# Kernel optimization log

Hardware: AMD Instinct MI355X
Metric: run time of the kernel (lower is better)

Reference implementation:

```python
import jax, jax.numpy as jnp
import numpy as np

# ---- dims (see shape_source) ----
N_NODES = 100_000
N_EDGES = 600_000
N_GRAPHS = 512
N_NODE_FEAT = 90   # atom-type vocabulary
H = 128            # n_hidden_feat
E_FEAT = 256       # n_edge_net_feat
G_FEAT = 128       # n_graph_feat
N_CONV = 3         # n_conv * n_edge_labels, conv_labels = [0,0,0]
SCALE = 0.05


def setup_inputs() -> dict:
    key = jax.random.key(0)
    ks = jax.random.split(key, 16)
    nodes = jax.random.randint(ks[0], (N_NODES,), 0, N_NODE_FEAT)
    edge_sources = jax.random.randint(ks[1], (N_EDGES,), 0, N_NODES)
    edge_targets = jax.random.randint(ks[2], (N_EDGES,), 0, N_NODES)
    graph_indices = jnp.sort(jax.random.randint(ks[3], (N_NODES,), 0, N_GRAPHS))
    node_counts = jnp.maximum(jnp.bincount(graph_indices, length=N_GRAPHS), 1).astype(jnp.float32)

    def rn(k, shape):
        return jax.random.normal(k, shape, jnp.float32) * SCALE

    return {
        "nodes": nodes,
        "edge_sources": edge_sources,
        "edge_targets": edge_targets,
        "graph_indices": graph_indices,
        "node_counts": node_counts,
        # learned parameters
        "embed": rn(ks[4], (N_NODE_FEAT, H)),           # NodeEmbedding table
        "Wg": rn(ks[5], (N_CONV, H, H)),                # gate linear per conv (bias=False)
        "We1": rn(ks[6], (N_CONV, H, E_FEAT)),          # EdgeNetwork layer 1 per conv
        "We2": rn(ks[7], (N_CONV, E_FEAT, H)),          # EdgeNetwork layer 2 per conv
        "Wp": rn(ks[8], (H, H)),                        # LinearPooling
        "Wfc1": rn(ks[9], (H, G_FEAT)), "bfc1": jnp.zeros((G_FEAT,), jnp.float32),
        "Wfc2": rn(ks[10], (G_FEAT, G_FEAT)), "bfc2": jnp.zeros((G_FEAT,), jnp.float32),
        "Wr": rn(ks[11], (G_FEAT, 1)), "br": jnp.zeros((1,), jnp.float32),
    }


def reference(nodes, edge_sources, edge_targets, graph_indices, node_counts,
              embed, Wg, We1, We2, Wp, Wfc1, bfc1, Wfc2, bfc2, Wr, br):
    sp = jax.nn.softplus
    # NodeEmbedding: atom-type lookup -> [N, H]
    x = embed[nodes]
    # Gated graph convolutions: gather -> edge MLP + gate -> scatter-add -> residual
    for i in range(N_CONV):
        z = x[edge_sources]                               # [E, H] gather
        e = sp(z @ We1[i]) @ We2[i]                       # EdgeNetwork (2 layers, no shortcut)
        m = jax.nn.sigmoid(z @ Wg[i]) * sp(e)             # gate * edge_activation(message)
        agg = jax.ops.segment_sum(m, edge_targets, num_segments=N_NODES)  # scatter-add
        x = x + sp(agg)                                   # node_activation + residual
    # LinearPooling (last conv only): per-graph mean of linear(x)
    y = jax.ops.segment_sum(x @ Wp, graph_indices, num_segments=N_GRAPHS) / node_counts[:, None]
    # GraphPooling with n_steps=1: activation only (no batch norm)
    g = sp(y)
    # FullConnection stack (n_fc=2)
    g = sp(g @ Wfc1 + bfc1)
    g = sp(g @ Wfc2 + bfc2)
    return g @ Wr + br
```

## Files before the change

kernel.cpp:

```cpp
#include <hip/hip_runtime.h>
#include <hip/hip_bf16.h>

typedef unsigned short u16;
typedef __attribute__((ext_vector_type(8))) short short8;
typedef __attribute__((ext_vector_type(4))) float f32x4;
typedef __attribute__((ext_vector_type(16))) float f32x16;
typedef __attribute__((ext_vector_type(2))) __bf16 bf16x2;

#define NNODES 100000
#define NEDGES 600000
#define NGRAPHS 512
#define HF 128
#define EF 256
#define GB 32

#define PLD 264
__device__ __forceinline__ int cidx(int chunk, int row){ return chunk * PLD + row * 8; }

__device__ __forceinline__ float bfu(u16 u){ return __uint_as_float(((unsigned)u) << 16); }
__device__ __forceinline__ u16 f2bf(float f){
    unsigned u = __float_as_uint(f);
    unsigned r = (u + 0x7fff + ((u >> 16) & 1)) >> 16;
    return (u16)r;
}
__device__ __forceinline__ unsigned pack2(float a, float b){
    bf16x2 v = { (__bf16)a, (__bf16)b };
    return __builtin_bit_cast(unsigned, v);
}

#if __has_builtin(__builtin_amdgcn_rcpf)
#define RCP1(x) __builtin_amdgcn_rcpf(x)
#else
#define RCP1(x) (1.f / (x))
#endif

__device__ __forceinline__ float sp_f(float x){
    return __logf(1.f + __expf(x));
}
__device__ __forceinline__ float sig_f(float x){
    return RCP1(1.f + __expf(-x));
}
__device__ __forceinline__ float lf(const void* p, long i, bool f32){
    return f32 ? ((const float*)p)[i] : bfu(((const u16*)p)[i]);
}

__device__ __forceinline__ bool is_f32(const void* probe){
    const u16* p = (const u16*)probe;
    int lane = threadIdx.x & 63;
    int c = 0;
#pragma unroll
    for (int i = 0; i < 4; i++) c += (fabsf(bfu(p[lane * 4 + i])) > 1.0f) ? 1 : 0;
#pragma unroll
    for (int off = 32; off; off >>= 1) c += __shfl_xor(c, off, 64);
    return c > 8;
}

__global__ __launch_bounds__(256) void prep_kernel(const void* __restrict__ wg,
                                                   const void* __restrict__ we1,
                                                   const void* __restrict__ we2,
                                                   const void* __restrict__ wp,
                                                   const void* __restrict__ wfc1,
                                                   const void* __restrict__ wfc2,
                                                   u16* __restrict__ pwg,
                                                   u16* __restrict__ pwe1,
                                                   u16* __restrict__ pwe2,
                                                   u16* __restrict__ pwp,
                                                   u16* __restrict__ pf1,
                                                   u16* __restrict__ pf2,
                                                   const void* __restrict__ emb,
                                                   const int* __restrict__ tgt,
                                                   int* __restrict__ counts,
                                                   float* __restrict__ xsum){
    int b = blockIdx.x, t = threadIdx.x;
    if (b < 960) {
        bool f32 = is_f32(emb);
        int i = b * 256 + t;
        int c = i / 81920, r = i % 81920;
        const void* src; u16* dst; int N, KN, l;
        if (r < 16384)      { src = wg;  dst = pwg;  N = HF; KN = 16384; l = r; }
        else if (r < 49152) { src = we1; dst = pwe1; N = EF; KN = 32768; l = r - 16384; }
        else                { src = we2; dst = pwe2; N = HF; KN = 32768; l = r - 49152; }
        int j = l & 7, lane = (l >> 3) & 63, rest = l >> 9;
        int NT = N >> 5;
        int nt = rest % NT, ks = rest / NT;
        int k = ks * 16 + (lane >> 5) * 8 + j;
        int n = nt * 32 + (lane & 31);
        long base = (long)c * KN;
        dst[base + l] = f2bf(lf(src, base + (long)k * N + n, f32));
    } else if (b < 1152) {
        bool f32 = is_f32(emb);
        int i = (b - 960) * 256 + t;
        int c = i / 16384, l = i % 16384;
        const void* src = (c == 0) ? wp : (c == 1) ? wfc1 : wfc2;
        u16* dst = (c == 0) ? pwp : (c == 1) ? pf1 : pf2;
        int j = l & 7, lane = (l >> 3) & 63, rest = l >> 9;
        int nt = rest & 7, kt = rest >> 3;
        int k = kt * 32 + (lane >> 4) * 8 + j;
        int n = nt * 16 + (lane & 15);
        dst[l] = f2bf(lf(src, (long)k * HF + n, f32));
    } else if (b < 3496) {
        int e = (b - 1152) * 256 + t;
        if (e < NEDGES) atomicAdd(&counts[tgt[e]], 1);
    } else {
        int i = (b - 3496) * 256 + t;
        ((float4*)xsum)[i] = make_float4(0.f, 0.f, 0.f, 0.f);
    }
}

__global__ __launch_bounds__(256) void scan1_kernel(const int* __restrict__ counts,
                                                    int* __restrict__ row_ptr,
                                                    int* __restrict__ bsums){
    __shared__ int s[256];
    int t = threadIdx.x;
    int i = blockIdx.x * 256 + t;
    int v = (i < NNODES) ? counts[i] : 0;
    s[t] = v; __syncthreads();
    for (int off = 1; off < 256; off <<= 1) {
        int a = (t >= off) ? s[t - off] : 0;
        __syncthreads();
        s[t] += a;
        __syncthreads();
    }
    if (i < NNODES) row_ptr[i] = s[t] - v;
    if (t == 255) bsums[blockIdx.x] = s[255];
}

__global__ __launch_bounds__(512) void scan2_kernel(const int* __restrict__ bsums,
                                                    int* __restrict__ boffs, int nb){
    __shared__ int s[512];
    int t = threadIdx.x;
    int v = (t < nb) ? bsums[t] : 0;
    s[t] = v; __syncthreads();
    for (int off = 1; off < 512; off <<= 1) {
        int a = (t >= off) ? s[t - off] : 0;
        __syncthreads();
        s[t] += a;
        __syncthreads();
    }
    if (t < nb) boffs[t] = s[t] - v;
}

__global__ __launch_bounds__(256) void scan3_kernel(int* __restrict__ row_ptr,
                                                    const int* __restrict__ boffs,
                                                    int* __restrict__ cursor){
    int i = blockIdx.x * 256 + threadIdx.x;
    if (i < NNODES) {
        int r = row_ptr[i] + boffs[blockIdx.x];
        row_ptr[i] = r;
        cursor[i]  = r;
    }
}

__global__ __launch_bounds__(256) void fill_kernel(const int* __restrict__ src,
                                                   const int* __restrict__ tgt,
                                                   int* __restrict__ cursor,
                                                   int* __restrict__ es){
    int e = blockIdx.x * 256 + threadIdx.x;
    if (e < NEDGES) {
        int pos = atomicAdd(&cursor[tgt[e]], 1);
        es[pos] = src[e];
    }
}

__device__ __forceinline__ void conv_phases(u16* xs, u16* us,
                                            const u16* __restrict__ pwg,
                                            const u16* __restrict__ pwe1,
                                            const u16* __restrict__ pwe2,
                                            u16* __restrict__ M, long row0){
    const int t = threadIdx.x;
    const int w = t >> 6, lane = t & 63;
    const int half = lane >> 5, nn = lane & 31;

    f32x16 acc0 = {}, acc1 = {};
#pragma unroll
    for (int ks = 0; ks < 8; ks++) {
        short8 A0 = *(const short8*)(pwe1 + (((ks * 8 + w) * 64 + lane) << 3));
        short8 A1 = *(const short8*)(pwe1 + (((ks * 8 + w + 4) * 64 + lane) << 3));
        short8 B  = *(const short8*)(&xs[cidx(ks * 2 + half, nn)]);
        acc0 = __builtin_amdgcn_mfma_f32_32x32x16_bf16(A0, B, acc0, 0, 0, 0);
        acc1 = __builtin_amdgcn_mfma_f32_32x32x16_bf16(A1, B, acc1, 0, 0, 0);
    }
#pragma unroll
    for (int q = 0; q < 4; q++) {
        uint2 d;
        d.x = pack2(sp_f(acc0[q*4+0]), sp_f(acc0[q*4+1]));
        d.y = pack2(sp_f(acc0[q*4+2]), sp_f(acc0[q*4+3]));
        *(uint2*)(&us[cidx(w * 4 + q, nn) + half * 4]) = d;
        uint2 e;
        e.x = pack2(sp_f(acc1[q*4+0]), sp_f(acc1[q*4+1]));
        e.y = pack2(sp_f(acc1[q*4+2]), sp_f(acc1[q*4+3]));
        *(uint2*)(&us[cidx(16 + w * 4 + q, nn) + half * 4]) = e;
    }
    __syncthreads();

    f32x16 aT = {};
#pragma unroll
    for (int jj = 0; jj < 16; jj++) {
        short8 Ac = *(const short8*)(pwe2 + (((jj * 4 + w) * 64 + lane) << 3));
        short8 B  = *(const short8*)(&us[cidx(jj * 2 + half, nn)]);
        aT = __builtin_amdgcn_mfma_f32_32x32x16_bf16(Ac, B, aT, 0, 0, 0);
    }

    f32x16 aG = {};
#pragma unroll
    for (int ks = 0; ks < 8; ks++) {
        short8 Ag = *(const short8*)(pwg + (((ks * 4 + w) * 64 + lane) << 3));
        short8 B  = *(const short8*)(&xs[cidx(ks * 2 + half, nn)]);
        aG = __builtin_amdgcn_mfma_f32_32x32x16_bf16(Ag, B, aG, 0, 0, 0);
    }
    long node = row0 + nn;
#pragma unroll
    for (int q = 0; q < 4; q++) {
        int h0 = w * 32 + half * 4 + q * 8;
        uint2 d;
        d.x = pack2(sig_f(aG[q*4+0]) * sp_f(aT[q*4+0]),
                    sig_f(aG[q*4+1]) * sp_f(aT[q*4+1]));
        d.y = pack2(sig_f(aG[q*4+2]) * sp_f(aT[q*4+2]),
                    sig_f(aG[q*4+3]) * sp_f(aT[q*4+3]));
        *(uint2*)(M + node * HF + h0) = d;
    }
}

__global__ __launch_bounds__(256, 6) void conv0_mfma(const int* __restrict__ nodes,
                                                     const void* __restrict__ emb,
                                                     u16* __restrict__ x,
                                                     const u16* __restrict__ pwg,
                                                     const u16* __restrict__ pwe1,
                                                     const u16* __restrict__ pwe2,
                                                     u16* __restrict__ M){
    __shared__ u16 xs[16 * PLD];
    __shared__ u16 us[32 * PLD];
    const int t = threadIdx.x;
    const long row0 = (long)blockIdx.x * 32;
    const bool f32 = is_f32(emb);

    for (int i = t; i < 512; i += 256) {
        int r = i >> 4, q = i & 15;
        long node = row0 + r;
        int v = nodes[node];
        uint4 d;
        if (f32) {
            float4 f0 = ((const float4*)emb)[(long)v * 32 + q * 2];
            float4 f1 = ((const float4*)emb)[(long)v * 32 + q * 2 + 1];
            d.x = pack2(f0.x, f0.y); d.y = pack2(f0.z, f0.w);
            d.z = pack2(f1.x, f1.y); d.w = pack2(f1.z, f1.w);
        } else {
            d = ((const uint4*)emb)[(long)v * 16 + q];
        }
        ((uint4*)x)[node * 16 + q] = d;
        *(uint4*)(&xs[cidx(q, r)]) = d;
    }
    __syncthreads();
    conv_phases(xs, us, pwg, pwe1, pwe2, M, row0);
}

__global__ __launch_bounds__(256, 6) void conv_mfma(const u16* __restrict__ x,
                                                    const u16* __restrict__ pwg,
                                                    const u16* __restrict__ pwe1,
                                                    const u16* __restrict__ pwe2,
                                                    u16* __restrict__ M){
    __shared__ u16 xs[16 * PLD];
    __shared__ u16 us[32 * PLD];
    const int t = threadIdx.x;
    const long row0 = (long)blockIdx.x * 32;

    for (int i = t; i < 512; i += 256) {
        int r = i >> 4, q = i & 15;
        long node = row0 + r;
        uint4 v = ((const uint4*)x)[node * 16 + q];
        *(uint4*)(&xs[cidx(q, r)]) = v;
    }
    __syncthreads();
    conv_phases(xs, us, pwg, pwe1, pwe2, M, row0);
}

__global__ __launch_bounds__(256) void agg_kernel(const u16* __restrict__ M,
                                                  const int* __restrict__ row_ptr,
                                                  const int* __restrict__ counts,
                                                  const int* __restrict__ es,
                                                  u16* __restrict__ x){
    int wid = blockIdx.x * 4 + (threadIdx.x >> 6);
    int lane = threadIdx.x & 63;
    long v = (long)wid * 4 + (lane >> 4);
    int l = lane & 15;
    if (v >= NNODES) return;
    int start = row_ptr[v], cnt = counts[v];
    float a0=0.f,a1=0.f,a2=0.f,a3=0.f,a4=0.f,a5=0.f,a6=0.f,a7=0.f;
    float b0=0.f,b1=0.f,b2=0.f,b3=0.f,b4=0.f,b5=0.f,b6=0.f,b7=0.f;
    const uint4* Mu = (const uint4*)M;
    int e = 0;
    for (; e + 3 < cnt; e += 4) {
        int s0 = es[start + e],     s1 = es[start + e + 1];
        int s2 = es[start + e + 2], s3 = es[start + e + 3];
        uint4 u0 = Mu[(long)s0 * 16 + l];
        uint4 u1 = Mu[(long)s1 * 16 + l];
        uint4 u2 = Mu[(long)s2 * 16 + l];
        uint4 u3 = Mu[(long)s3 * 16 + l];
        a0 += bfu((u16)u0.x); a1 += bfu((u16)(u0.x >> 16));
        a2 += bfu((u16)u0.y); a3 += bfu((u16)(u0.y >> 16));
        a4 += bfu((u16)u0.z); a5 += bfu((u16)(u0.z >> 16));
        a6 += bfu((u16)u0.w); a7 += bfu((u16)(u0.w >> 16));
        b0 += bfu((u16)u1.x); b1 += bfu((u16)(u1.x >> 16));
        b2 += bfu((u16)u1.y); b3 += bfu((u16)(u1.y >> 16));
        b4 += bfu((u16)u1.z); b5 += bfu((u16)(u1.z >> 16));
        b6 += bfu((u16)u1.w); b7 += bfu((u16)(u1.w >> 16));
        a0 += bfu((u16)u2.x); a1 += bfu((u16)(u2.x >> 16));
        a2 += bfu((u16)u2.y); a3 += bfu((u16)(u2.y >> 16));
        a4 += bfu((u16)u2.z); a5 += bfu((u16)(u2.z >> 16));
        a6 += bfu((u16)u2.w); a7 += bfu((u16)(u2.w >> 16));
        b0 += bfu((u16)u3.x); b1 += bfu((u16)(u3.x >> 16));
        b2 += bfu((u16)u3.y); b3 += bfu((u16)(u3.y >> 16));
        b4 += bfu((u16)u3.z); b5 += bfu((u16)(u3.z >> 16));
        b6 += bfu((u16)u3.w); b7 += bfu((u16)(u3.w >> 16));
    }
    for (; e < cnt; e++) {
        int s0 = es[start + e];
        uint4 u0 = Mu[(long)s0 * 16 + l];
        a0 += bfu((u16)u0.x); a1 += bfu((u16)(u0.x >> 16));
        a2 += bfu((u16)u0.y); a3 += bfu((u16)(u0.y >> 16));
        a4 += bfu((u16)u0.z); a5 += bfu((u16)(u0.z >> 16));
        a6 += bfu((u16)u0.w); a7 += bfu((u16)(u0.w >> 16));
    }
    a0 += b0; a1 += b1; a2 += b2; a3 += b3;
    a4 += b4; a5 += b5; a6 += b6; a7 += b7;
    uint4* xu = (uint4*)x;
    uint4 xv = xu[v * 16 + l];
    xv.x = pack2(bfu((u16)xv.x) + sp_f(a0), bfu((u16)(xv.x >> 16)) + sp_f(a1));
    xv.y = pack2(bfu((u16)xv.y) + sp_f(a2), bfu((u16)(xv.y >> 16)) + sp_f(a3));
    xv.z = pack2(bfu((u16)xv.z) + sp_f(a4), bfu((u16)(xv.z >> 16)) + sp_f(a5));
    xv.w = pack2(bfu((u16)xv.w) + sp_f(a6), bfu((u16)(xv.w >> 16)) + sp_f(a7));
    xu[v * 16 + l] = xv;
}

__global__ __launch_bounds__(256) void pool_kernel(const u16* __restrict__ x,
                                                   const int* __restrict__ gidx,
                                                   float* __restrict__ xsum){
    int wave = blockIdx.x * 4 + (threadIdx.x >> 6);
    int lane = threadIdx.x & 63;
    long base = (long)wave * 64;
    if (base >= NNODES) return;
    long end = base + 64; if (end > NNODES) end = NNODES;
    const unsigned* xu = (const unsigned*)x;
    int gcur = gidx[base];
    float a0 = 0.f, a1 = 0.f;
    for (long v = base; v < end; v++) {
        int g = gidx[v];
        if (g != gcur) {
            atomicAdd(&xsum[gcur * HF + lane * 2 + 0], a0);
            atomicAdd(&xsum[gcur * HF + lane * 2 + 1], a1);
            a0 = a1 = 0.f; gcur = g;
        }
        unsigned u = xu[v * 64 + lane];
        a0 += bfu((u16)u);
        a1 += bfu((u16)(u >> 16));
    }
    atomicAdd(&xsum[gcur * HF + lane * 2 + 0], a0);
    atomicAdd(&xsum[gcur * HF + lane * 2 + 1], a1);
}

__global__ __launch_bounds__(256) void head_mfma(const float* __restrict__ xsum,
                                                 const void* __restrict__ ncnt,
                                                 const u16* __restrict__ pwp,
                                                 const u16* __restrict__ pf1,
                                                 const u16* __restrict__ pf2,
                                                 const void* __restrict__ bfc1,
                                                 const void* __restrict__ bfc2,
                                                 const void* __restrict__ Wr,
                                                 const void* __restrict__ br,
                                                 void* __restrict__ out,
                                                 const void* __restrict__ probe){
    __shared__ u16 hibuf[2][GB][136];
    __shared__ u16 lobuf[2][GB][136];
    const int t = threadIdx.x;
    const int w = t >> 6, lane = t & 63;
    const int quad = lane >> 4, nr = lane & 15;
    const bool f32 = is_f32(probe);
    const int g0 = blockIdx.x * GB;

    for (int i = t; i < GB * 64; i += 256) {
        int g = i >> 6, c = (i & 63) * 2;
        float f0 = xsum[(g0 + g) * HF + c], f1 = xsum[(g0 + g) * HF + c + 1];
        u16 h0 = f2bf(f0), h1 = f2bf(f1);
        *(unsigned*)&hibuf[0][g][c] = (unsigned)h0 | ((unsigned)h1 << 16);
        *(unsigned*)&lobuf[0][g][c] = pack2(f0 - bfu(h0), f1 - bfu(h1));
    }
    __syncthreads();

    float rc[2];
#pragma unroll
    for (int nt = 0; nt < 2; nt++) rc[nt] = RCP1(lf(ncnt, g0 + nt * 16 + nr, f32));

    int cur = 0;
    for (int layer = 0; layer < 3; layer++) {
        const u16* pw = (layer == 0) ? pwp : (layer == 1) ? pf1 : pf2;
        const void* bias = (layer == 1) ? bfc1 : bfc2;
        int nxt = cur ^ 1;
#pragma unroll
        for (int c = 0; c < 2; c++) {
            int et = w * 2 + c;
            short8 A[4];
#pragma unroll
            for (int kt = 0; kt < 4; kt++)
                A[kt] = *(const short8*)(pw + (((kt * 8 + et) * 64 + lane) << 3));
#pragma unroll
            for (int nt = 0; nt < 2; nt++) {
                f32x4 acc = {0.f, 0.f, 0.f, 0.f};
#pragma unroll
                for (int kt = 0; kt < 4; kt++) {
                    short8 bh = *(const short8*)(&hibuf[cur][nt * 16 + nr][kt * 32 + quad * 8]);
                    short8 bl = *(const short8*)(&lobuf[cur][nt * 16 + nr][kt * 32 + quad * 8]);
                    acc = __builtin_amdgcn_mfma_f32_16x16x32_bf16(A[kt], bh, acc, 0, 0, 0);
                    acc = __builtin_amdgcn_mfma_f32_16x16x32_bf16(A[kt], bl, acc, 0, 0, 0);
                }
                int feat0 = et * 16 + quad * 4;
                float f[4];
#pragma unroll
                for (int r = 0; r < 4; r++) {
                    float a = (layer == 0) ? acc[r] * rc[nt]
                                           : acc[r] + lf(bias, feat0 + r, f32);
                    f[r] = sp_f(a);
                }
                u16 h[4]; float lo[4];
#pragma unroll
                for (int r = 0; r < 4; r++) { h[r] = f2bf(f[r]); lo[r] = f[r] - bfu(h[r]); }
                uint2 dh, dl;
                dh.x = (unsigned)h[0] | ((unsigned)h[1] << 16);
                dh.y = (unsigned)h[2] | ((unsigned)h[3] << 16);
                dl.x = pack2(lo[0], lo[1]);
                dl.y = pack2(lo[2], lo[3]);
                *(uint2*)&hibuf[nxt][nt * 16 + nr][feat0] = dh;
                *(uint2*)&lobuf[nxt][nt * 16 + nr][feat0] = dl;
            }
        }
        __syncthreads();
        cur = nxt;
    }

    int g = t >> 3, sub = t & 7;
    float p = 0.f;
    for (int k = sub * 16; k < sub * 16 + 16; k++) {
        float v = bfu(hibuf[cur][g][k]) + bfu(lobuf[cur][g][k]);
        p += v * lf(Wr, k, f32);
    }
    p += __shfl_down(p, 4, 64);
    p += __shfl_down(p, 2, 64);
    p += __shfl_down(p, 1, 64);
    if (sub == 0) {
        float res = p + lf(br, 0, f32);
        if (f32) ((float*)out)[g0 + g] = res;
        else     ((u16*)out)[g0 + g]  = f2bf(res);
    }
}

extern "C" void kernel_launch(void* const* d_in, const int* in_sizes, int n_in,
                              void* d_out, int out_size, void* d_ws, size_t ws_size,
                              hipStream_t stream) {
    const int* nodes = (const int*)d_in[0];
    const int* esrc  = (const int*)d_in[1];
    const int* etgt  = (const int*)d_in[2];
    const int* gidx  = (const int*)d_in[3];

    size_t off = 0;
    char* w = (char*)d_ws;
    auto take = [&](size_t bytes) -> void* {
        void* p = w + off;
        off = (off + bytes + 255) & ~(size_t)255;
        return p;
    };

    u16* pwg     = (u16*)take((size_t)3 * HF * HF * 2);
    u16* pwe1    = (u16*)take((size_t)3 * HF * EF * 2);
    u16* pwe2    = (u16*)take((size_t)3 * EF * HF * 2);
    u16* pwp     = (u16*)take((size_t)HF * HF * 2);
    u16* pf1     = (u16*)take((size_t)HF * HF * 2);
    u16* pf2     = (u16*)take((size_t)HF * HF * 2);
    int* counts  = (int*)take((size_t)NNODES * 4);
    int* row_ptr = (int*)take((size_t)NNODES * 4);
    int* cursor  = (int*)take((size_t)NNODES * 4);
    int* es      = (int*)take((size_t)NEDGES * 4);
    int* bsums   = (int*)take(2048);
    int* boffs   = (int*)take(2048);
    float* xsum  = (float*)take((size_t)NGRAPHS * HF * 4);
    u16* x       = (u16*)take((size_t)NNODES * HF * 2);
    u16* M       = (u16*)take((size_t)NNODES * HF * 2);

    hipMemsetAsync(counts, 0, (size_t)NNODES * 4, stream);

    prep_kernel<<<3560, 256, 0, stream>>>(d_in[6], d_in[7], d_in[8],
                                          d_in[9], d_in[10], d_in[12],
                                          pwg, pwe1, pwe2, pwp, pf1, pf2,
                                          d_in[5], etgt, counts, xsum);

    const int NB_SCAN = (NNODES + 255) / 256;
    const int NB_EDGE = (NEDGES + 255) / 256;
    scan1_kernel<<<NB_SCAN, 256, 0, stream>>>(counts, row_ptr, bsums);
    scan2_kernel<<<1, 512, 0, stream>>>(bsums, boffs, NB_SCAN);
    scan3_kernel<<<NB_SCAN, 256, 0, stream>>>(row_ptr, boffs, cursor);
    fill_kernel<<<NB_EDGE, 256, 0, stream>>>(esrc, etgt, cursor, es);

    const int NBC = (NNODES + 31) / 32;
    const int NBA = (NNODES + 15) / 16;
    conv0_mfma<<<NBC, 256, 0, stream>>>(nodes, d_in[5], x, pwg, pwe1, pwe2, M);
    agg_kernel<<<NBA, 256, 0, stream>>>(M, row_ptr, counts, es, x);
    conv_mfma<<<NBC, 256, 0, stream>>>(x,
        pwg + (size_t)1 * HF * HF, pwe1 + (size_t)1 * HF * EF, pwe2 + (size_t)1 * EF * HF, M);
    agg_kernel<<<NBA, 256, 0, stream>>>(M, row_ptr, counts, es, x);
    conv_mfma<<<NBC, 256, 0, stream>>>(x,
        pwg + (size_t)2 * HF * HF, pwe1 + (size_t)2 * HF * EF, pwe2 + (size_t)2 * EF * HF, M);
    agg_kernel<<<NBA, 256, 0, stream>>>(M, row_ptr, counts, es, x);

    pool_kernel<<<(NNODES + 255) / 256, 256, 0, stream>>>(x, gidx, xsum);
    head_mfma<<<NGRAPHS / GB, 256, 0, stream>>>(xsum, d_in[4], pwp, pf1, pf2,
                                                d_in[11], d_in[13], d_in[14], d_in[15],
                                                d_out, d_in[5]);
}
```

Baseline: 392.6 us.

## Make conv kernels persistent with register-resident weights and prefetched node tiles

Measured after the change: 388.0 us. Within noise of the previous version (-1.2%).

```diff
diff --git a/kernel.cpp b/kernel.cpp
--- a/kernel.cpp
+++ b/kernel.cpp
@@ -13,6 +13,8 @@
 #define HF 128
 #define EF 256
 #define GB 32
+#define NTILES 3125
+#define GRID_CONV 512
 
 #define PLD 264
 __device__ __forceinline__ int cidx(int chunk, int row){ return chunk * PLD + row * 8; }
@@ -162,23 +164,33 @@
     }
 }
 
-__device__ __forceinline__ void conv_phases(u16* xs, u16* us,
-                                            const u16* __restrict__ pwg,
-                                            const u16* __restrict__ pwe1,
-                                            const u16* __restrict__ pwe2,
-                                            u16* __restrict__ M, long row0){
-    const int t = threadIdx.x;
-    const int w = t >> 6, lane = t & 63;
+struct ConvW { short8 wu0[8], wu1[8], wc[16], wg[8]; };
+
+__device__ __forceinline__ void load_w(ConvW& W, const u16* __restrict__ pwg,
+                                       const u16* __restrict__ pwe1,
+                                       const u16* __restrict__ pwe2,
+                                       int w, int lane){
+#pragma unroll
+    for (int ks = 0; ks < 8; ks++) {
+        W.wu0[ks] = *(const short8*)(pwe1 + (((ks * 8 + w) * 64 + lane) << 3));
+        W.wu1[ks] = *(const short8*)(pwe1 + (((ks * 8 + w + 4) * 64 + lane) << 3));
+        W.wg[ks]  = *(const short8*)(pwg  + (((ks * 4 + w) * 64 + lane) << 3));
+    }
+#pragma unroll
+    for (int jj = 0; jj < 16; jj++)
+        W.wc[jj] = *(const short8*)(pwe2 + (((jj * 4 + w) * 64 + lane) << 3));
+}
+
+__device__ __forceinline__ void conv_loop1(const ConvW& W, const u16* xs, u16* us,
+                                           int w, int lane, f32x16& aG_out){
     const int half = lane >> 5, nn = lane & 31;
-
-    f32x16 acc0 = {}, acc1 = {};
+    f32x16 acc0 = {}, acc1 = {}, g = {};
 #pragma unroll
     for (int ks = 0; ks < 8; ks++) {
-        short8 A0 = *(const short8*)(pwe1 + (((ks * 8 + w) * 64 + lane) << 3));
-        short8 A1 = *(const short8*)(pwe1 + (((ks * 8 + w + 4) * 64 + lane) << 3));
-        short8 B  = *(const short8*)(&xs[cidx(ks * 2 + half, nn)]);
-        acc0 = __builtin_amdgcn_mfma_f32_32x32x16_bf16(A0, B, acc0, 0, 0, 0);
-        acc1 = __builtin_amdgcn_mfma_f32_32x32x16_bf16(A1, B, acc1, 0, 0, 0);
+        short8 B = *(const short8*)(&xs[cidx(ks * 2 + half, nn)]);
+        acc0 = __builtin_amdgcn_mfma_f32_32x32x16_bf16(W.wu0[ks], B, acc0, 0, 0, 0);
+        acc1 = __builtin_amdgcn_mfma_f32_32x32x16_bf16(W.wu1[ks], B, acc1, 0, 0, 0);
+        g    = __builtin_amdgcn_mfma_f32_32x32x16_bf16(W.wg[ks],  B, g,    0, 0, 0);
     }
 #pragma unroll
     for (int q = 0; q < 4; q++) {
@@ -191,22 +203,18 @@
         e.y = pack2(sp_f(acc1[q*4+2]), sp_f(acc1[q*4+3]));
         *(uint2*)(&us[cidx(16 + w * 4 + q, nn) + half * 4]) = e;
     }
-    __syncthreads();
-
+    aG_out = g;
+}
+
+__device__ __forceinline__ void conv_loop2(const ConvW& W, const u16* us,
+                                           const f32x16& aG, u16* __restrict__ M,
+                                           long row0, int w, int lane){
+    const int half = lane >> 5, nn = lane & 31;
     f32x16 aT = {};
 #pragma unroll
     for (int jj = 0; jj < 16; jj++) {
-        short8 Ac = *(const short8*)(pwe2 + (((jj * 4 + w) * 64 + lane) << 3));
-        short8 B  = *(const short8*)(&us[cidx(jj * 2 + half, nn)]);
-        aT = __builtin_amdgcn_mfma_f32_32x32x16_bf16(Ac, B, aT, 0, 0, 0);
-    }
-
-    f32x16 aG = {};
-#pragma unroll
-    for (int ks = 0; ks < 8; ks++) {
-        short8 Ag = *(const short8*)(pwg + (((ks * 4 + w) * 64 + lane) << 3));
-        short8 B  = *(const short8*)(&xs[cidx(ks * 2 + half, nn)]);
-        aG = __builtin_amdgcn_mfma_f32_32x32x16_bf16(Ag, B, aG, 0, 0, 0);
+        short8 B = *(const short8*)(&us[cidx(jj * 2 + half, nn)]);
+        aT = __builtin_amdgcn_mfma_f32_32x32x16_bf16(W.wc[jj], B, aT, 0, 0, 0);
     }
     long node = row0 + nn;
 #pragma unroll
@@ -221,7 +229,7 @@
     }
 }
 
-__global__ __launch_bounds__(256, 6) void conv0_mfma(const int* __restrict__ nodes,
+__global__ __launch_bounds__(256, 2) void conv0_mfma(const int* __restrict__ nodes,
                                                      const void* __restrict__ emb,
                                                      u16* __restrict__ x,
                                                      const u16* __restrict__ pwg,
@@ -231,30 +239,82 @@
     __shared__ u16 xs[16 * PLD];
     __shared__ u16 us[32 * PLD];
     const int t = threadIdx.x;
-    const long row0 = (long)blockIdx.x * 32;
+    const int w = t >> 6, lane = t & 63;
+    const int r0 = t >> 4, q = t & 15;
     const bool f32 = is_f32(emb);
 
-    for (int i = t; i < 512; i += 256) {
-        int r = i >> 4, q = i & 15;
-        long node = row0 + r;
-        int v = nodes[node];
-        uint4 d;
+    ConvW W;
+    load_w(W, pwg, pwe1, pwe2, w, lane);
+
+    const float4* ef = (const float4*)emb;
+    const uint4*  eu = (const uint4*)emb;
+    uint4* xg = (uint4*)x;
+
+    int tile = blockIdx.x;
+    {
+        long row0 = (long)tile * 32;
+        int v0 = nodes[row0 + r0], v1 = nodes[row0 + r0 + 16];
+        uint4 b0, b1;
         if (f32) {
-            float4 f0 = ((const float4*)emb)[(long)v * 32 + q * 2];
-            float4 f1 = ((const float4*)emb)[(long)v * 32 + q * 2 + 1];
-            d.x = pack2(f0.x, f0.y); d.y = pack2(f0.z, f0.w);
-            d.z = pack2(f1.x, f1.y); d.w = pack2(f1.z, f1.w);
+            float4 f0 = ef[(long)v0 * 32 + q * 2], f1 = ef[(long)v0 * 32 + q * 2 + 1];
+            float4 f2 = ef[(long)v1 * 32 + q * 2], f3 = ef[(long)v1 * 32 + q * 2 + 1];
+            b0.x = pack2(f0.x, f0.y); b0.y = pack2(f0.z, f0.w);
+            b0.z = pack2(f1.x, f1.y); b0.w = pack2(f1.z, f1.w);
+            b1.x = pack2(f2.x, f2.y); b1.y = pack2(f2.z, f2.w);
+            b1.z = pack2(f3.x, f3.y); b1.w = pack2(f3.z, f3.w);
         } else {
-            d = ((const uint4*)emb)[(long)v * 16 + q];
+            b0 = eu[(long)v0 * 16 + q];
+            b1 = eu[(long)v1 * 16 + q];
         }
-        ((uint4*)x)[node * 16 + q] = d;
-        *(uint4*)(&xs[cidx(q, r)]) = d;
+        xg[(row0 + r0) * 16 + q] = b0;
+        xg[(row0 + r0 + 16) * 16 + q] = b1;
+        *(uint4*)(&xs[cidx(q, r0)]) = b0;
+        *(uint4*)(&xs[cidx(q, r0 + 16)]) = b1;
     }
     __syncthreads();
-    conv_phases(xs, us, pwg, pwe1, pwe2, M, row0);
-}
-
-__global__ __launch_bounds__(256, 6) void conv_mfma(const u16* __restrict__ x,
+
+    for (;;) {
+        long row0 = (long)tile * 32;
+        int nxt = tile + GRID_CONV;
+        bool have = nxt < NTILES;
+        uint4 nb0 = {}, nb1 = {};
+        float4 nf0 = {}, nf1 = {}, nf2 = {}, nf3 = {};
+        if (have) {
+            long nr = (long)nxt * 32;
+            int v0 = nodes[nr + r0], v1 = nodes[nr + r0 + 16];
+            if (f32) {
+                nf0 = ef[(long)v0 * 32 + q * 2]; nf1 = ef[(long)v0 * 32 + q * 2 + 1];
+                nf2 = ef[(long)v1 * 32 + q * 2]; nf3 = ef[(long)v1 * 32 + q * 2 + 1];
+            } else {
+                nb0 = eu[(long)v0 * 16 + q];
+                nb1 = eu[(long)v1 * 16 + q];
+            }
+        }
+        f32x16 aG;
+        conv_loop1(W, xs, us, w, lane, aG);
+        __syncthreads();
+        if (have) {
+            uint4 b0 = nb0, b1 = nb1;
+            if (f32) {
+                b0.x = pack2(nf0.x, nf0.y); b0.y = pack2(nf0.z, nf0.w);
+                b0.z = pack2(nf1.x, nf1.y); b0.w = pack2(nf1.z, nf1.w);
+                b1.x = pack2(nf2.x, nf2.y); b1.y = pack2(nf2.z, nf2.w);
+                b1.z = pack2(nf3.x, nf3.y); b1.w = pack2(nf3.z, nf3.w);
+            }
+            long nr = (long)nxt * 32;
+            xg[(nr + r0) * 16 + q] = b0;
+            xg[(nr + r0 + 16) * 16 + q] = b1;
+            *(uint4*)(&xs[cidx(q, r0)]) = b0;
+            *(uint4*)(&xs[cidx(q, r0 + 16)]) = b1;
+        }
+        conv_loop2(W, us, aG, M, row0, w, lane);
+        if (!have) break;
+        __syncthreads();
+        tile = nxt;
+    }
+}
+
+__global__ __launch_bounds__(256, 2) void conv_mfma(const u16* __restrict__ x,
                                                     const u16* __restrict__ pwg,
                                                     const u16* __restrict__ pwe1,
                                                     const u16* __restrict__ pwe2,
@@ -262,16 +322,45 @@
     __shared__ u16 xs[16 * PLD];
     __shared__ u16 us[32 * PLD];
     const int t = threadIdx.x;
-    const long row0 = (long)blockIdx.x * 32;
-
-    for (int i = t; i < 512; i += 256) {
-        int r = i >> 4, q = i & 15;
-        long node = row0 + r;
-        uint4 v = ((const uint4*)x)[node * 16 + q];
-        *(uint4*)(&xs[cidx(q, r)]) = v;
+    const int w = t >> 6, lane = t & 63;
+    const int r0 = t >> 4, q = t & 15;
+
+    ConvW W;
+    load_w(W, pwg, pwe1, pwe2, w, lane);
+
+    const uint4* xg = (const uint4*)x;
+    int tile = blockIdx.x;
+    {
+        long row0 = (long)tile * 32;
+        uint4 b0 = xg[(row0 + r0) * 16 + q];
+        uint4 b1 = xg[(row0 + r0 + 16) * 16 + q];
+        *(uint4*)(&xs[cidx(q, r0)]) = b0;
+        *(uint4*)(&xs[cidx(q, r0 + 16)]) = b1;
     }
     __syncthreads();
-    conv_phases(xs, us, pwg, pwe1, pwe2, M, row0);
+
+    for (;;) {
+        long row0 = (long)tile * 32;
+        int nxt = tile + GRID_CONV;
+        bool have = nxt < NTILES;
+        uint4 nb0 = {}, nb1 = {};
+        if (have) {
+            long nr = (long)nxt * 32;
+            nb0 = xg[(nr + r0) * 16 + q];
+            nb1 = xg[(nr + r0 + 16) * 16 + q];
+        }
+        f32x16 aG;
+        conv_loop1(W, xs, us, w, lane, aG);
+        __syncthreads();
+        if (have) {
+            *(uint4*)(&xs[cidx(q, r0)]) = nb0;
+            *(uint4*)(&xs[cidx(q, r0 + 16)]) = nb1;
+        }
+        conv_loop2(W, us, aG, M, row0, w, lane);
+        if (!have) break;
+        __syncthreads();
+        tile = nxt;
+    }
 }
 
 __global__ __launch_bounds__(256) void agg_kernel(const u16* __restrict__ M,
@@ -498,14 +587,13 @@
     scan3_kernel<<<NB_SCAN, 256, 0, stream>>>(row_ptr, boffs, cursor);
     fill_kernel<<<NB_EDGE, 256, 0, stream>>>(esrc, etgt, cursor, es);
 
-    const int NBC = (NNODES + 31) / 32;
     const int NBA = (NNODES + 15) / 16;
-    conv0_mfma<<<NBC, 256, 0, stream>>>(nodes, d_in[5], x, pwg, pwe1, pwe2, M);
+    conv0_mfma<<<GRID_CONV, 256, 0, stream>>>(nodes, d_in[5], x, pwg, pwe1, pwe2, M);
     agg_kernel<<<NBA, 256, 0, stream>>>(M, row_ptr, counts, es, x);
-    conv_mfma<<<NBC, 256, 0, stream>>>(x,
+    conv_mfma<<<GRID_CONV, 256, 0, stream>>>(x,
         pwg + (size_t)1 * HF * HF, pwe1 + (size_t)1 * HF * EF, pwe2 + (size_t)1 * EF * HF, M);
     agg_kernel<<<NBA, 256, 0, stream>>>(M, row_ptr, counts, es, x);
-    conv_mfma<<<NBC, 256, 0, stream>>>(x,
+    conv_mfma<<<GRID_CONV, 256, 0, stream>>>(x,
         pwg + (size_t)2 * HF * HF, pwe1 + (size_t)2 * HF * EF, pwe2 + (size_t)2 * EF * HF, M);
     agg_kernel<<<NBA, 256, 0, stream>>>(M, row_ptr, counts, es, x);
 
```

## Run conv tiles on a single wave with register-resident activations, no LDS

Applied to the files above, without the earlier changes.

After: 433.4 us. 1.1x slower.

```diff
diff --git a/kernel.cpp b/kernel.cpp
--- a/kernel.cpp
+++ b/kernel.cpp
@@ -13,9 +13,7 @@
 #define HF 128
 #define EF 256
 #define GB 32
-
-#define PLD 264
-__device__ __forceinline__ int cidx(int chunk, int row){ return chunk * PLD + row * 8; }
+#define NTILES 3125
 
 __device__ __forceinline__ float bfu(u16 u){ return __uint_as_float(((unsigned)u) << 16); }
 __device__ __forceinline__ u16 f2bf(float f){
@@ -162,116 +160,118 @@
     }
 }
 
-__device__ __forceinline__ void conv_phases(u16* xs, u16* us,
-                                            const u16* __restrict__ pwg,
-                                            const u16* __restrict__ pwe1,
-                                            const u16* __restrict__ pwe2,
-                                            u16* __restrict__ M, long row0){
-    const int t = threadIdx.x;
-    const int w = t >> 6, lane = t & 63;
-    const int half = lane >> 5, nn = lane & 31;
-
-    f32x16 acc0 = {}, acc1 = {};
-#pragma unroll
-    for (int ks = 0; ks < 8; ks++) {
-        short8 A0 = *(const short8*)(pwe1 + (((ks * 8 + w) * 64 + lane) << 3));
-        short8 A1 = *(const short8*)(pwe1 + (((ks * 8 + w + 4) * 64 + lane) << 3));
-        short8 B  = *(const short8*)(&xs[cidx(ks * 2 + half, nn)]);
-        acc0 = __builtin_amdgcn_mfma_f32_32x32x16_bf16(A0, B, acc0, 0, 0, 0);
-        acc1 = __builtin_amdgcn_mfma_f32_32x32x16_bf16(A1, B, acc1, 0, 0, 0);
-    }
-#pragma unroll
-    for (int q = 0; q < 4; q++) {
-        uint2 d;
-        d.x = pack2(sp_f(acc0[q*4+0]), sp_f(acc0[q*4+1]));
-        d.y = pack2(sp_f(acc0[q*4+2]), sp_f(acc0[q*4+3]));
-        *(uint2*)(&us[cidx(w * 4 + q, nn) + half * 4]) = d;
-        uint2 e;
-        e.x = pack2(sp_f(acc1[q*4+0]), sp_f(acc1[q*4+1]));
-        e.y = pack2(sp_f(acc1[q*4+2]), sp_f(acc1[q*4+3]));
-        *(uint2*)(&us[cidx(16 + w * 4 + q, nn) + half * 4]) = e;
-    }
-    __syncthreads();
-
-    f32x16 aT = {};
-#pragma unroll
-    for (int jj = 0; jj < 16; jj++) {
-        short8 Ac = *(const short8*)(pwe2 + (((jj * 4 + w) * 64 + lane) << 3));
-        short8 B  = *(const short8*)(&us[cidx(jj * 2 + half, nn)]);
-        aT = __builtin_amdgcn_mfma_f32_32x32x16_bf16(Ac, B, aT, 0, 0, 0);
-    }
-
-    f32x16 aG = {};
-#pragma unroll
-    for (int ks = 0; ks < 8; ks++) {
-        short8 Ag = *(const short8*)(pwg + (((ks * 4 + w) * 64 + lane) << 3));
-        short8 B  = *(const short8*)(&xs[cidx(ks * 2 + half, nn)]);
-        aG = __builtin_amdgcn_mfma_f32_32x32x16_bf16(Ag, B, aG, 0, 0, 0);
-    }
-    long node = row0 + nn;
-#pragma unroll
-    for (int q = 0; q < 4; q++) {
-        int h0 = w * 32 + half * 4 + q * 8;
-        uint2 d;
-        d.x = pack2(sig_f(aG[q*4+0]) * sp_f(aT[q*4+0]),
-                    sig_f(aG[q*4+1]) * sp_f(aT[q*4+1]));
-        d.y = pack2(sig_f(aG[q*4+2]) * sp_f(aT[q*4+2]),
-                    sig_f(aG[q*4+3]) * sp_f(aT[q*4+3]));
-        *(uint2*)(M + node * HF + h0) = d;
-    }
-}
-
-__global__ __launch_bounds__(256, 6) void conv0_mfma(const int* __restrict__ nodes,
-                                                     const void* __restrict__ emb,
-                                                     u16* __restrict__ x,
-                                                     const u16* __restrict__ pwg,
-                                                     const u16* __restrict__ pwe1,
-                                                     const u16* __restrict__ pwe2,
-                                                     u16* __restrict__ M){
-    __shared__ u16 xs[16 * PLD];
-    __shared__ u16 us[32 * PLD];
-    const int t = threadIdx.x;
-    const long row0 = (long)blockIdx.x * 32;
-    const bool f32 = is_f32(emb);
-
-    for (int i = t; i < 512; i += 256) {
-        int r = i >> 4, q = i & 15;
-        long node = row0 + r;
-        int v = nodes[node];
-        uint4 d;
-        if (f32) {
-            float4 f0 = ((const float4*)emb)[(long)v * 32 + q * 2];
-            float4 f1 = ((const float4*)emb)[(long)v * 32 + q * 2 + 1];
-            d.x = pack2(f0.x, f0.y); d.y = pack2(f0.z, f0.w);
-            d.z = pack2(f1.x, f1.y); d.w = pack2(f1.z, f1.w);
-        } else {
-            d = ((const uint4*)emb)[(long)v * 16 + q];
-        }
-        ((uint4*)x)[node * 16 + q] = d;
-        *(uint4*)(&xs[cidx(q, r)]) = d;
-    }
-    __syncthreads();
-    conv_phases(xs, us, pwg, pwe1, pwe2, M, row0);
-}
-
-__global__ __launch_bounds__(256, 6) void conv_mfma(const u16* __restrict__ x,
+__device__ __forceinline__ void conv_core(const uint4* xf,
+                                          const u16* __restrict__ pwg,
+                                          const u16* __restrict__ pwe1,
+                                          const u16* __restrict__ pwe2,
+                                          u16* __restrict__ M,
+                                          long node, int lane){
+    const int h = lane >> 5;
+
+    uint4 BU[16];
+#pragma unroll
+    for (int et = 0; et < 8; et++) {
+        f32x16 acc = {};
+#pragma unroll
+        for (int ks = 0; ks < 8; ks++) {
+            short8 A = *(const short8*)(pwe1 + (((ks * 8 + et) * 64 + lane) << 3));
+            acc = __builtin_amdgcn_mfma_f32_32x32x16_bf16(
+                      A, __builtin_bit_cast(short8, xf[ks]), acc, 0, 0, 0);
+        }
+#pragma unroll
+        for (int rb = 0; rb < 2; rb++) {
+            unsigned a1 = pack2(sp_f(acc[rb*8+0]), sp_f(acc[rb*8+1]));
+            unsigned a2 = pack2(sp_f(acc[rb*8+2]), sp_f(acc[rb*8+3]));
+            unsigned b1 = pack2(sp_f(acc[rb*8+4]), sp_f(acc[rb*8+5]));
+            unsigned b2 = pack2(sp_f(acc[rb*8+6]), sp_f(acc[rb*8+7]));
+            unsigned t1 = __shfl_xor(h ? a1 : b1, 32, 64);
+            unsigned t2 = __shfl_xor(h ? a2 : b2, 32, 64);
+            BU[et*2+rb] = make_uint4(h ? t1 : a1, h ? t2 : a2,
+                                     h ? b1 : t1, h ? b2 : t2);
+        }
+    }
+
+#pragma unroll 1
+    for (int ht = 0; ht < 4; ht++) {
+        f32x16 aT = {};
+#pragma unroll
+        for (int jj = 0; jj < 16; jj++) {
+            short8 A = *(const short8*)(pwe2 + (((jj * 4 + ht) * 64 + lane) << 3));
+            aT = __builtin_amdgcn_mfma_f32_32x32x16_bf16(
+                     A, __builtin_bit_cast(short8, BU[jj]), aT, 0, 0, 0);
+        }
+        f32x16 aG = {};
+#pragma unroll
+        for (int ks = 0; ks < 8; ks++) {
+            short8 A = *(const short8*)(pwg + (((ks * 4 + ht) * 64 + lane) << 3));
+            aG = __builtin_amdgcn_mfma_f32_32x32x16_bf16(
+                     A, __builtin_bit_cast(short8, xf[ks]), aG, 0, 0, 0);
+        }
+#pragma unroll
+        for (int q = 0; q < 4; q++) {
+            int h0 = ht * 32 + h * 4 + q * 8;
+            uint2 d;
+            d.x = pack2(sig_f(aG[q*4+0]) * sp_f(aT[q*4+0]),
+                        sig_f(aG[q*4+1]) * sp_f(aT[q*4+1]));
+            d.y = pack2(sig_f(aG[q*4+2]) * sp_f(aT[q*4+2]),
+                        sig_f(aG[q*4+3]) * sp_f(aT[q*4+3]));
+            *(uint2*)(M + node * HF + h0) = d;
+        }
+    }
+}
+
+__global__ __launch_bounds__(64, 2) void conv0_mfma(const int* __restrict__ nodes,
+                                                    const void* __restrict__ emb,
+                                                    u16* __restrict__ x,
                                                     const u16* __restrict__ pwg,
                                                     const u16* __restrict__ pwe1,
                                                     const u16* __restrict__ pwe2,
                                                     u16* __restrict__ M){
-    __shared__ u16 xs[16 * PLD];
-    __shared__ u16 us[32 * PLD];
-    const int t = threadIdx.x;
-    const long row0 = (long)blockIdx.x * 32;
-
-    for (int i = t; i < 512; i += 256) {
-        int r = i >> 4, q = i & 15;
-        long node = row0 + r;
-        uint4 v = ((const uint4*)x)[node * 16 + q];
-        *(uint4*)(&xs[cidx(q, r)]) = v;
-    }
-    __syncthreads();
-    conv_phases(xs, us, pwg, pwe1, pwe2, M, row0);
+    const int lane = threadIdx.x;
+    const int h = lane >> 5, nn = lane & 31;
+    const long node = (long)blockIdx.x * 32 + nn;
+    const bool f32 = is_f32(emb);
+    const int v = nodes[node];
+
+    uint4 xf[8];
+    if (f32) {
+        const float4* ef = (const float4*)emb;
+#pragma unroll
+        for (int ks = 0; ks < 8; ks++) {
+            float4 f0 = ef[(long)v * 32 + ks * 4 + h * 2];
+            float4 f1 = ef[(long)v * 32 + ks * 4 + h * 2 + 1];
+            uint4 d;
+            d.x = pack2(f0.x, f0.y); d.y = pack2(f0.z, f0.w);
+            d.z = pack2(f1.x, f1.y); d.w = pack2(f1.z, f1.w);
+            xf[ks] = d;
+        }
+    } else {
+        const uint4* eu = (const uint4*)emb;
+#pragma unroll
+        for (int ks = 0; ks < 8; ks++) xf[ks] = eu[(long)v * 16 + ks * 2 + h];
+    }
+    uint4* xg = (uint4*)x;
+#pragma unroll
+    for (int ks = 0; ks < 8; ks++) xg[node * 16 + ks * 2 + h] = xf[ks];
+
+    conv_core(xf, pwg, pwe1, pwe2, M, node, lane);
+}
+
+__global__ __launch_bounds__(64, 2) void conv_mfma(const u16* __restrict__ x,
+                                                   const u16* __restrict__ pwg,
+                                                   const u16* __restrict__ pwe1,
+                                                   const u16* __restrict__ pwe2,
+                                                   u16* __restrict__ M){
+    const int lane = threadIdx.x;
+    const int h = lane >> 5, nn = lane & 31;
+    const long node = (long)blockIdx.x * 32 + nn;
+    const uint4* xg = (const uint4*)x;
+
+    uint4 xf[8];
+#pragma unroll
+    for (int ks = 0; ks < 8; ks++) xf[ks] = xg[node * 16 + ks * 2 + h];
+
+    conv_core(xf, pwg, pwe1, pwe2, M, node, lane);
 }
 
 __global__ __launch_bounds__(256) void agg_kernel(const u16* __restrict__ M,
@@ -498,14 +498,13 @@
     scan3_kernel<<<NB_SCAN, 256, 0, stream>>>(row_ptr, boffs, cursor);
     fill_kernel<<<NB_EDGE, 256, 0, stream>>>(esrc, etgt, cursor, es);
 
-    const int NBC = (NNODES + 31) / 32;
     const int NBA = (NNODES + 15) / 16;
-    conv0_mfma<<<NBC, 256, 0, stream>>>(nodes, d_in[5], x, pwg, pwe1, pwe2, M);
+    conv0_mfma<<<NTILES, 64, 0, stream>>>(nodes, d_in[5], x, pwg, pwe1, pwe2, M);
     agg_kernel<<<NBA, 256, 0, stream>>>(M, row_ptr, counts, es, x);
-    conv_mfma<<<NBC, 256, 0, stream>>>(x,
+    conv_mfma<<<NTILES, 64, 0, stream>>>(x,
         pwg + (size_t)1 * HF * HF, pwe1 + (size_t)1 * HF * EF, pwe2 + (size_t)1 * EF * HF, M);
     agg_kernel<<<NBA, 256, 0, stream>>>(M, row_ptr, counts, es, x);
-    conv_mfma<<<NBC, 256, 0, stream>>>(x,
+    conv_mfma<<<NTILES, 64, 0, stream>>>(x,
         pwg + (size_t)2 * HF * HF, pwe1 + (size_t)2 * HF * EF, pwe2 + (size_t)2 * EF * HF, M);
     agg_kernel<<<NBA, 256, 0, stream>>>(M, row_ptr, counts, es, x);
 
```
